# Performance work log

Hardware: AMD Instinct MI355X
Metric: run time of the kernel (lower is better)

## Reference

```python
import jax, jax.numpy as jnp
from jax import lax
import numpy as np

NPOINT = 1024
RADIUS = 0.25
NSAMPLE = 32
USE_XYZ = True


def setup_inputs() -> dict:
    key = jax.random.key(0)
    k1, k2 = jax.random.split(key)
    xyz = jax.random.normal(k1, (8, 8192, 3), dtype=jnp.float32)
    points = jax.random.normal(k2, (8, 8192, 32), dtype=jnp.float32)
    return {"xyz": xyz, "points": points}


def furthest_point_sample(xyz, npoint):
    """Iterative FPS; returns (B, npoint, 3) sampled coordinates.
    Matches torch reference: seeded with xyz[:, 0], squared-distance metric."""
    B, N, _ = xyz.shape
    first = xyz[:, 0]  # (B, 3)
    d0 = jnp.full((B, N), 1e38, dtype=xyz.dtype)

    def step(carry, _):
        dist, last = carry  # dist: (B,N), last: (B,3)
        d2 = jnp.sum((xyz - last[:, None, :]) ** 2, axis=-1)  # (B,N)
        dist = jnp.minimum(dist, d2)
        idx = jnp.argmax(dist, axis=1)  # (B,)
        nxt = jnp.take_along_axis(xyz, idx[:, None, None], axis=1)[:, 0]  # (B,3)
        return (dist, nxt), nxt

    _, outs = lax.scan(step, (d0, first), None, length=npoint - 1)  # (npoint-1, B, 3)
    return jnp.concatenate([first[None], outs], axis=0).transpose(1, 0, 2)  # (B,npoint,3)


def ball_query(radius, nsample, xyz, new_xyz):
    """First `nsample` indices within `radius` of each center (ascending index
    order), padded with the first found index — matches pointnet2 CUDA kernel.
    Returns (B, npoint, nsample) int32."""
    N = xyz.shape[1]
    d2 = jnp.sum((new_xyz[:, :, None, :] - xyz[:, None, :, :]) ** 2, axis=-1)  # (B,npoint,N)
    mask = d2 < radius * radius
    ar = jnp.arange(N, dtype=jnp.int32)
    # top_k on negated indices -> smallest valid indices first
    score = jnp.where(mask, -ar, jnp.int32(-(N + 1)))
    vals, _ = lax.top_k(score, nsample)  # (B,npoint,nsample), descending
    valid = vals > -(N + 1)
    idx = jnp.where(valid, -vals, -vals[..., :1])  # pad with first hit
    return idx.astype(jnp.int32)


def group_points(points, idx):
    """points (B,N,C), idx (B,npoint,nsample) -> (B,npoint,nsample,C)."""
    B, npoint, nsample = idx.shape
    C = points.shape[-1]
    flat = idx.reshape(B, npoint * nsample)  # (B, npoint*nsample)
    g = jnp.take_along_axis(points, flat[:, :, None], axis=1)
    return g.reshape(B, npoint, nsample, C)


def reference(xyz, points):
    new_xyz = furthest_point_sample(xyz, NPOINT)  # (B,npoint,3)
    idx = ball_query(RADIUS, NSAMPLE, xyz, new_xyz)  # (B,npoint,nsample)
    grouped_xyz = group_points(xyz, idx) - new_xyz[:, :, None, :]  # center-relative
    grouped_points = group_points(points, idx)
    if USE_XYZ:
        new_points = jnp.concatenate([grouped_xyz, grouped_points], axis=-1)
    else:
        new_points = grouped_points
    return new_xyz, new_points
```

## Files before the change

### kernel.cpp

```cpp
#include <hip/hip_runtime.h>

#define BATCH   8
#define NPTS    8192
#define NPOINT  1024
#define NSAMPLE 32
#define CHANC   32
#define OUTC    35
#define R2      0.0625f

typedef float v2f __attribute__((ext_vector_type(2)));

template <int CTRL>
__device__ __forceinline__ float dpp_max_step(float v) {
    int r = __builtin_amdgcn_update_dpp(__float_as_int(v), __float_as_int(v),
                                        CTRL, 0xf, 0xf, false);
    return fmaxf(v, __int_as_float(r));
}
#define DPP_ROW_SHR(n)  (0x110 | (n))
#define DPP_BCAST15     0x142
#define DPP_BCAST31     0x143

__global__ __launch_bounds__(512) void fps_kernel(const float* __restrict__ xyz,
                                                  float* __restrict__ new_xyz) {
#pragma clang fp contract(off)
    const int b    = blockIdx.x;
    const int t    = threadIdx.x;
    const int lane = t & 63;
    const int w    = t >> 6;
    const float* bx = xyz + (size_t)b * NPTS * 3;

    __shared__ float4 pts[NPTS];
    __shared__ unsigned long long partial[2][8];

    v2f px[8], py[8], pz[8], dist[8];
    {
        float f[48];
        float4* fq = (float4*)f;
        const float4* s4 = (const float4*)bx + t * 12;
#pragma unroll
        for (int q = 0; q < 12; ++q) fq[q] = s4[q];
#pragma unroll
        for (int p = 0; p < 8; ++p) {
            px[p] = (v2f){f[6 * p + 0], f[6 * p + 3]};
            py[p] = (v2f){f[6 * p + 1], f[6 * p + 4]};
            pz[p] = (v2f){f[6 * p + 2], f[6 * p + 5]};
            dist[p] = (v2f){1e38f, 1e38f};
        }
#pragma unroll
        for (int i = 0; i < 16; ++i) {
            const int j  = t * 16 + i;
            const int js = j ^ ((j >> 4) & 7);
            pts[js] = make_float4(f[3 * i + 0], f[3 * i + 1], f[3 * i + 2], 0.0f);
        }
    }
    __syncthreads();

    float4 c0 = pts[0];
    float lx = c0.x, ly = c0.y, lz = c0.z;
    if (t == 0) {
        float* o = new_xyz + (size_t)b * NPOINT * 3;
        o[0] = lx; o[1] = ly; o[2] = lz;
    }

    for (int s = 1; s < NPOINT; ++s) {
        const v2f lx2 = (v2f){lx, lx};
        const v2f ly2 = (v2f){ly, ly};
        const v2f lz2 = (v2f){lz, lz};
        float bestv = -1.0f;
        int   bi    = 0;
#pragma unroll
        for (int p = 0; p < 8; ++p) {
            const v2f dx = px[p] - lx2;
            const v2f dy = py[p] - ly2;
            const v2f dz = pz[p] - lz2;
            const v2f d2 = (dx * dx + dy * dy) + dz * dz;
            const float d0 = fminf(dist[p].x, d2.x);
            const float d1 = fminf(dist[p].y, d2.y);
            dist[p] = (v2f){d0, d1};
            if (d0 > bestv) { bestv = d0; bi = 2 * p; }
            if (d1 > bestv) { bestv = d1; bi = 2 * p + 1; }
        }
        const int besti = (t << 4) + bi;

        float v = bestv;
        v = dpp_max_step<DPP_ROW_SHR(1)>(v);
        v = dpp_max_step<DPP_ROW_SHR(2)>(v);
        v = dpp_max_step<DPP_ROW_SHR(4)>(v);
        v = dpp_max_step<DPP_ROW_SHR(8)>(v);
        v = dpp_max_step<DPP_BCAST15>(v);
        v = dpp_max_step<DPP_BCAST31>(v);
        const float smax = __int_as_float(__builtin_amdgcn_readlane(__float_as_int(v), 63));

        const unsigned long long m = __ballot(bestv == smax);
        const int par = s & 1;
        if (lane == (int)__builtin_ctzll(m)) {
            partial[par][w] = ((unsigned long long)__float_as_uint(smax) << 32)
                              | (unsigned)(~besti);
        }
        __syncthreads();

        unsigned long long bp = partial[par][0];
#pragma unroll
        for (int q = 1; q < 8; ++q) {
            const unsigned long long o = partial[par][q];
            if (o > bp) bp = o;
        }
        const int idx = (int)(~(unsigned)bp);
        const int js  = idx ^ ((idx >> 4) & 7);
        const float4 c = pts[js];
        lx = c.x; ly = c.y; lz = c.z;
        if (t == 0) {
            float* o = new_xyz + ((size_t)b * NPOINT + s) * 3;
            o[0] = lx; o[1] = ly; o[2] = lz;
        }
    }
}

__global__ __launch_bounds__(256) void ballgroup_kernel(const float* __restrict__ xyz,
                                                        const float* __restrict__ points,
                                                        const float* __restrict__ new_xyz,
                                                        float* __restrict__ out) {
#pragma clang fp contract(off)
    const int lane = threadIdx.x & 63;
    const int w    = threadIdx.x >> 6;
    const int gw   = blockIdx.x * 4 + w;
    const int b    = gw >> 10;

    const float* bx  = xyz + (size_t)b * NPTS * 3;
    const float* cen = new_xyz + (size_t)gw * 3;
    const float cx = cen[0], cy = cen[1], cz = cen[2];

    __shared__ int idxbuf[4][NSAMPLE];

    int k = 0;
    for (int base = 0; base < NPTS; base += 64) {
        const int j = base + lane;
        const float dx = bx[j * 3 + 0] - cx;
        const float dy = bx[j * 3 + 1] - cy;
        const float dz = bx[j * 3 + 2] - cz;
        const float d2 = (dx * dx + dy * dy) + dz * dz;
        const bool in = d2 < R2;
        const unsigned long long mask = __ballot(in);
        const int pre = __popcll(mask & ((1ull << lane) - 1ull));
        if (in && (k + pre) < NSAMPLE) idxbuf[w][k + pre] = j;
        k += __popcll(mask);
        if (k >= NSAMPLE) { k = NSAMPLE; break; }
    }
    const int first = idxbuf[w][0];

    float*       o    = out + (size_t)gw * NSAMPLE * OUTC;
    const float* prow = points + (size_t)b * NPTS * CHANC;
    for (int e = lane; e < NSAMPLE * OUTC; e += 64) {
        const int s = e / OUTC;
        const int c = e - s * OUTC;
        const int j = (s < k) ? idxbuf[w][s] : first;
        float v;
        if (c < 3) {
            const float cc = (c == 0) ? cx : (c == 1) ? cy : cz;
            v = bx[j * 3 + c] - cc;
        } else {
            v = prow[j * CHANC + (c - 3)];
        }
        o[e] = v;
    }
}

extern "C" void kernel_launch(void* const* d_in, const int* in_sizes, int n_in,
                              void* d_out, int out_size, void* d_ws, size_t ws_size,
                              hipStream_t stream) {
    const float* xyz    = (const float*)d_in[0];
    const float* points = (const float*)d_in[1];
    float* new_xyz    = (float*)d_out;
    float* new_points = new_xyz + (size_t)BATCH * NPOINT * 3;

    fps_kernel<<<BATCH, 512, 0, stream>>>(xyz, new_xyz);
    ballgroup_kernel<<<(BATCH * NPOINT) / 4, 256, 0, stream>>>(xyz, points, new_xyz, new_points);
}
```

Baseline: 1.022 ms.

## Pack two batches per FPS block, drop LDS point cache, unroll ball query

The FPS kernel now runs two batches per 512-thread block, with 256 threads per batch each holding 32 points in registers. This halves the grid and removes the shared-memory copy of the points. The selected point's coordinates are now read from global memory instead of LDS. The ball-query scan loads two 64-point chunks per iteration to expose more memory-level parallelism. The trade-off is double the per-thread distance work on the sequential FPS critical path, fewer active CUs, and a global load in each step's dependency chain.

New measurement: 1.736 ms. 69.9% more time.

```diff
diff --git a/kernel.cpp b/kernel.cpp
--- a/kernel.cpp
+++ b/kernel.cpp
@@ -23,41 +23,34 @@
 __global__ __launch_bounds__(512) void fps_kernel(const float* __restrict__ xyz,
                                                   float* __restrict__ new_xyz) {
 #pragma clang fp contract(off)
-    const int b    = blockIdx.x;
     const int t    = threadIdx.x;
+    const int team = t >> 8;
+    const int tt   = t & 255;
     const int lane = t & 63;
-    const int w    = t >> 6;
+    const int w    = (t >> 6) & 3;
+    const int b    = blockIdx.x * 2 + team;
     const float* bx = xyz + (size_t)b * NPTS * 3;
 
-    __shared__ float4 pts[NPTS];
-    __shared__ unsigned long long partial[2][8];
+    __shared__ unsigned long long partial[2][2][4];
 
-    v2f px[8], py[8], pz[8], dist[8];
+    v2f px[16], py[16], pz[16], dist[16];
     {
-        float f[48];
+        float f[96];
         float4* fq = (float4*)f;
-        const float4* s4 = (const float4*)bx + t * 12;
+        const float4* s4 = (const float4*)bx + tt * 24;
 #pragma unroll
-        for (int q = 0; q < 12; ++q) fq[q] = s4[q];
+        for (int q = 0; q < 24; ++q) fq[q] = s4[q];
 #pragma unroll
-        for (int p = 0; p < 8; ++p) {
+        for (int p = 0; p < 16; ++p) {
             px[p] = (v2f){f[6 * p + 0], f[6 * p + 3]};
             py[p] = (v2f){f[6 * p + 1], f[6 * p + 4]};
             pz[p] = (v2f){f[6 * p + 2], f[6 * p + 5]};
             dist[p] = (v2f){1e38f, 1e38f};
         }
-#pragma unroll
-        for (int i = 0; i < 16; ++i) {
-            const int j  = t * 16 + i;
-            const int js = j ^ ((j >> 4) & 7);
-            pts[js] = make_float4(f[3 * i + 0], f[3 * i + 1], f[3 * i + 2], 0.0f);
-        }
     }
-    __syncthreads();
 
-    float4 c0 = pts[0];
-    float lx = c0.x, ly = c0.y, lz = c0.z;
-    if (t == 0) {
+    float lx = bx[0], ly = bx[1], lz = bx[2];
+    if (tt == 0) {
         float* o = new_xyz + (size_t)b * NPOINT * 3;
         o[0] = lx; o[1] = ly; o[2] = lz;
     }
@@ -69,7 +62,7 @@
         float bestv = -1.0f;
         int   bi    = 0;
 #pragma unroll
-        for (int p = 0; p < 8; ++p) {
+        for (int p = 0; p < 16; ++p) {
             const v2f dx = px[p] - lx2;
             const v2f dy = py[p] - ly2;
             const v2f dz = pz[p] - lz2;
@@ -80,7 +73,7 @@
             if (d0 > bestv) { bestv = d0; bi = 2 * p; }
             if (d1 > bestv) { bestv = d1; bi = 2 * p + 1; }
         }
-        const int besti = (t << 4) + bi;
+        const int besti = (tt << 5) + bi;
 
         float v = bestv;
         v = dpp_max_step<DPP_ROW_SHR(1)>(v);
@@ -94,22 +87,22 @@
         const unsigned long long m = __ballot(bestv == smax);
         const int par = s & 1;
         if (lane == (int)__builtin_ctzll(m)) {
-            partial[par][w] = ((unsigned long long)__float_as_uint(smax) << 32)
-                              | (unsigned)(~besti);
+            partial[par][team][w] = ((unsigned long long)__float_as_uint(smax) << 32)
+                                    | (unsigned)(~besti);
         }
         __syncthreads();
 
-        unsigned long long bp = partial[par][0];
+        unsigned long long bp = partial[par][team][0];
 #pragma unroll
-        for (int q = 1; q < 8; ++q) {
-            const unsigned long long o = partial[par][q];
+        for (int q = 1; q < 4; ++q) {
+            const unsigned long long o = partial[par][team][q];
             if (o > bp) bp = o;
         }
         const int idx = (int)(~(unsigned)bp);
-        const int js  = idx ^ ((idx >> 4) & 7);
-        const float4 c = pts[js];
-        lx = c.x; ly = c.y; lz = c.z;
-        if (t == 0) {
+
+        const float* wp = bx + idx * 3;
+        lx = wp[0]; ly = wp[1]; lz = wp[2];
+        if (tt == 0) {
             float* o = new_xyz + ((size_t)b * NPOINT + s) * 3;
             o[0] = lx; o[1] = ly; o[2] = lz;
         }
@@ -133,17 +126,28 @@
     __shared__ int idxbuf[4][NSAMPLE];
 
     int k = 0;
-    for (int base = 0; base < NPTS; base += 64) {
-        const int j = base + lane;
-        const float dx = bx[j * 3 + 0] - cx;
-        const float dy = bx[j * 3 + 1] - cy;
-        const float dz = bx[j * 3 + 2] - cz;
-        const float d2 = (dx * dx + dy * dy) + dz * dz;
-        const bool in = d2 < R2;
-        const unsigned long long mask = __ballot(in);
-        const int pre = __popcll(mask & ((1ull << lane) - 1ull));
-        if (in && (k + pre) < NSAMPLE) idxbuf[w][k + pre] = j;
-        k += __popcll(mask);
+    for (int base = 0; base < NPTS; base += 128) {
+        const int j0 = base + lane;
+        const int j1 = j0 + 64;
+        const float a0 = bx[j0 * 3 + 0], a1 = bx[j0 * 3 + 1], a2 = bx[j0 * 3 + 2];
+        const float c0 = bx[j1 * 3 + 0], c1 = bx[j1 * 3 + 1], c2 = bx[j1 * 3 + 2];
+        const float dxa = a0 - cx, dya = a1 - cy, dza = a2 - cz;
+        const float d2a = (dxa * dxa + dya * dya) + dza * dza;
+        const float dxb = c0 - cx, dyb = c1 - cy, dzb = c2 - cz;
+        const float d2b = (dxb * dxb + dyb * dyb) + dzb * dzb;
+        const bool inA = d2a < R2;
+        const bool inB = d2b < R2;
+
+        const unsigned long long mA = __ballot(inA);
+        int pre = __popcll(mA & ((1ull << lane) - 1ull));
+        if (inA && (k + pre) < NSAMPLE) idxbuf[w][k + pre] = j0;
+        k += __popcll(mA);
+        if (k >= NSAMPLE) { k = NSAMPLE; break; }
+
+        const unsigned long long mB = __ballot(inB);
+        pre = __popcll(mB & ((1ull << lane) - 1ull));
+        if (inB && (k + pre) < NSAMPLE) idxbuf[w][k + pre] = j1;
+        k += __popcll(mB);
         if (k >= NSAMPLE) { k = NSAMPLE; break; }
     }
     const int first = idxbuf[w][0];
@@ -173,6 +177,6 @@
     float* new_xyz    = (float*)d_out;
     float* new_points = new_xyz + (size_t)BATCH * NPOINT * 3;
 
-    fps_kernel<<<BATCH, 512, 0, stream>>>(xyz, new_xyz);
+    fps_kernel<<<BATCH / 2, 512, 0, stream>>>(xyz, new_xyz);
     ballgroup_kernel<<<(BATCH * NPOINT) / 4, 256, 0, stream>>>(xyz, points, new_xyz, new_points);
 }
```
